# Performance work log

Measured on AMD Instinct MI355X. Metric: run time of the kernel, lower is better.

Reference implementation:

```python
import jax, jax.numpy as jnp
import numpy as np


def _lstm_cell(x, h, c, W_ih, W_hh, b_ih, b_hh):
    # torch.nn.LSTMCell math; gate order i, f, g, o
    gates = x @ W_ih.T + b_ih + h @ W_hh.T + b_hh
    i, f, g, o = jnp.split(gates, 4, axis=-1)
    c_new = jax.nn.sigmoid(f) * c + jax.nn.sigmoid(i) * jnp.tanh(g)
    h_new = jax.nn.sigmoid(o) * jnp.tanh(c_new)
    return h_new, c_new


def setup_inputs() -> dict:
    key = jax.random.key(0)
    ks = jax.random.split(key, 14)
    B, T, F = 16384, 128, 12
    H1, H2 = 64, 128
    s0 = 1.0 / np.sqrt(H1)
    s1 = 1.0 / np.sqrt(H2)
    u = lambda k, shape, s: jax.random.uniform(k, shape, jnp.float32, -s, s)
    return {
        "input_seq": jax.random.normal(ks[0], (B, T, F), jnp.float32),
        "W_ih0": u(ks[1], (4 * H1, F), s0),
        "W_hh0": u(ks[2], (4 * H1, H1), s0),
        "b_ih0": u(ks[3], (4 * H1,), s0),
        "b_hh0": u(ks[4], (4 * H1,), s0),
        "W_ih1": u(ks[5], (4 * H2, H1), s1),
        "W_hh1": u(ks[6], (4 * H2, H2), s1),
        "b_ih1": u(ks[7], (4 * H2,), s1),
        "b_hh1": u(ks[8], (4 * H2,), s1),
        "W_d1": u(ks[9], (H1, H2), s1),
        "b_d1": u(ks[10], (H1,), s1),
        "W_d2": u(ks[11], (1, H1), s0),
        "b_d2": u(ks[12], (1,), s0),
    }


def reference(input_seq, W_ih0, W_hh0, b_ih0, b_hh0,
              W_ih1, W_hh1, b_ih1, b_hh1,
              W_d1, b_d1, W_d2, b_d2):
    B = input_seq.shape[0]
    H1 = W_hh0.shape[1]
    H2 = W_hh1.shape[1]
    dt = input_seq.dtype
    init = (jnp.zeros((B, H1), dt), jnp.zeros((B, H1), dt),
            jnp.zeros((B, H2), dt), jnp.zeros((B, H2), dt))

    def step(carry, x_t):
        h0, c0, h1, c1 = carry
        h0, c0 = _lstm_cell(x_t, h0, c0, W_ih0, W_hh0, b_ih0, b_hh0)
        # dropout is identity in eval mode
        h1, c1 = _lstm_cell(h0, h1, c1, W_ih1, W_hh1, b_ih1, b_hh1)
        return (h0, c0, h1, c1), None

    xs = jnp.swapaxes(input_seq, 0, 1)  # [T, B, F]
    (h0, c0, h1, c1), _ = jax.lax.scan(step, init, xs)
    pred = (h1 @ W_d1.T + b_d1) @ W_d2.T + b_d2  # [B, 1]
    return pred
```

## Files before the change

kernel.cpp:

```cpp
#include <hip/hip_runtime.h>
#include <hip/hip_fp16.h>


#define T_STEPS 128
#define F_IN    12
#define R       32

#define WF0_H8  (16*3*64)
#define WF1_H8  (16*12*64)
#define WH_TOTAL_HALVES ((WF0_H8 + WF1_H8)*8)

typedef _Float16 half8 __attribute__((ext_vector_type(8)));
typedef _Float16 half4 __attribute__((ext_vector_type(4)));
typedef float   floatx4  __attribute__((ext_vector_type(4)));
typedef float   floatx16 __attribute__((ext_vector_type(16)));
typedef int     intx4  __attribute__((ext_vector_type(4)));

__device__ __forceinline__ float vexp2(float x){
  float r; asm("v_exp_f32 %0, %1" : "=v"(r) : "v"(x)); return r;
}
__device__ __forceinline__ float vrcp(float x){
  float r; asm("v_rcp_f32 %0, %1" : "=v"(r) : "v"(x)); return r;
}
__device__ __forceinline__ float sigf(float x){
  return vrcp(1.0f + vexp2(-1.4426950408889634f * x));
}
__device__ __forceinline__ float tanhf_(float x){
  return fmaf(2.0f, vrcp(1.0f + vexp2(-2.8853900817779268f * x)), -1.0f);
}

__device__ __forceinline__ float qpx1(float v){
  return __int_as_float(__builtin_amdgcn_update_dpp(
      0, __float_as_int(v), 0xB1 , 0xF, 0xF, true));
}
__device__ __forceinline__ float qpx2(float v){
  return __int_as_float(__builtin_amdgcn_update_dpp(
      0, __float_as_int(v), 0x4E , 0xF, 0xF, true));
}
__device__ __forceinline__ floatx4 qtrans4(floatx4 s, int g){
  float e0 = qpx1(s[1]), e1 = qpx1(s[0]), e2 = qpx1(s[3]), e3 = qpx1(s[2]);
  const bool lo = (g & 1);
  float m0 = lo ? e0   : s[0];
  float m1 = lo ? s[1] : e1;
  float m2 = lo ? e2   : s[2];
  float m3 = lo ? s[3] : e3;
  float f0 = qpx2(m2), f1 = qpx2(m3), f2 = qpx2(m0), f3 = qpx2(m1);
  const bool hi = (g & 2);
  floatx4 d;
  d[0] = hi ? f0 : m0;
  d[1] = hi ? f1 : m1;
  d[2] = hi ? m2 : f2;
  d[3] = hi ? m3 : f3;
  return d;
}

__global__ void prep_kernel(const float* __restrict__ Wih0, const float* __restrict__ Whh0,
                            const float* __restrict__ bih0, const float* __restrict__ bhh0,
                            const float* __restrict__ Wih1, const float* __restrict__ Whh1,
                            const float* __restrict__ bih1, const float* __restrict__ bhh1,
                            _Float16* __restrict__ wh, float* __restrict__ bs) {
  int tid = blockIdx.x * 256 + threadIdx.x;
  if (tid < WF0_H8) {
    int lane = tid & 63; int kt = (tid >> 6) % 3; int ct = tid / (64*3);
    int p = ct*16 + (lane & 15);
    int col = (p & 3)*64 + (p >> 2);
    int kbase = kt*32 + (lane >> 4)*8;
    #pragma unroll
    for (int j = 0; j < 8; ++j) {
      int k = kbase + j; float w = 0.0f;
      if (k < 12) w = Wih0[col*12 + k];
      else if (k < 76) w = Whh0[col*64 + (k-12)];
      wh[tid*8 + j] = (_Float16)w;
    }
  } else if (tid < WF0_H8 + WF1_H8) {
    int t2 = tid - WF0_H8;
    int lane = t2 & 63; int kt = (t2 >> 6) % 12; int ct = t2 / (64*12);
    int p = ct*32 + (lane & 31);
    int col = (p & 3)*128 + (p >> 2);
    int kbase = kt*16 + (lane >> 5)*8;
    #pragma unroll
    for (int j = 0; j < 8; ++j) {
      int k = kbase + j;
      float w = (k < 64) ? Wih1[col*64 + k] : Whh1[col*128 + (k-64)];
      wh[WF0_H8*8 + t2*8 + j] = (_Float16)w;
    }
  } else if (tid < WF0_H8 + WF1_H8 + 768) {
    int t3 = tid - (WF0_H8 + WF1_H8);
    if (t3 < 256) { int col = (t3 & 3)*64 + (t3 >> 2);  bs[t3] = bih0[col] + bhh0[col]; }
    else { int p1 = t3 - 256; int col = (p1 & 3)*128 + (p1 >> 2); bs[t3] = bih1[col] + bhh1[col]; }
  }
}

__global__ __launch_bounds__(512, 1)
void lstm_kernel(const float* __restrict__ x, const _Float16* __restrict__ wh,
                 const float* __restrict__ bs,
                 const float* __restrict__ Wd1, const float* __restrict__ bd1,
                 const float* __restrict__ Wd2, const float* __restrict__ bd2,
                 float* __restrict__ out) {
  __shared__ __align__(16) _Float16 st0[2*R*128];
  __shared__ __align__(16) _Float16 st1[R*512];
  __shared__ float hbuf[R*132];
  __shared__ float red[R*17];

  const int tid  = threadIdx.x;
  const int w    = tid >> 6;
  const int lane = tid & 63;
  const int l15  = lane & 15;
  const int l31  = lane & 31;
  const int lg   = lane >> 4;
  const int hi5  = lane >> 5;
  const int qg   = lane & 3;
  const int a    = l15 >> 2;
  const int r    = lg*4 + qg;
  const int rowbase = blockIdx.x * R;

  auto st0a = [](int buf, int row, int blk){
    return (buf*R + row)*128 + (((blk ^ (row & 7)) << 3)); };
  auto st0s = [](int buf, int row, int idx){
    return (buf*R + row)*128 + ((((idx >> 3) ^ (row & 7)) << 3) | (idx & 7)); };
  auto st1a = [](int row, int blk){
    return row*512 + (((blk ^ (row & 7)) << 3)); };
  auto st1s = [](int row, int idx){
    return row*512 + ((((idx >> 3) ^ (row & 7)) << 3) | (idx & 7)); };

  const intx4* whi = (const intx4*)wh;
  intx4 wb0i[2][3];
  #pragma unroll
  for (int i = 0; i < 2; ++i)
    #pragma unroll
    for (int kt = 0; kt < 3; ++kt) wb0i[i][kt] = whi[((2*w+i)*3 + kt)*64 + lane];
  intx4 wb1i[2][12];
  #pragma unroll
  for (int i = 0; i < 2; ++i)
    #pragma unroll
    for (int kt = 0; kt < 12; ++kt) wb1i[i][kt] = whi[WF0_H8 + ((2*w+i)*12 + kt)*64 + lane];
  float b0[2], b1[2];
  #pragma unroll
  for (int i = 0; i < 2; ++i) b0[i] = bs[(2*w+i)*16 + l15];
  #pragma unroll
  for (int i = 0; i < 2; ++i) b1[i] = bs[256 + (2*w+i)*32 + l31];

  float c0s[2][2] = {{0.0f,0.0f},{0.0f,0.0f}};
  float c1s[2][4] = {{0.0f,0.0f,0.0f,0.0f},{0.0f,0.0f,0.0f,0.0f}};

  for (int i = tid; i < (2*R*128)/2; i += 512) ((int*)st0)[i] = 0;
  for (int i = tid; i < (R*512)/2;   i += 512) ((int*)st1)[i] = 0;
  __syncthreads();
  const int xr = tid / 3, xq = tid % 3;
  if (tid < 96) {
    float4 v0 = *(const float4*)&x[((size_t)(rowbase + xr)*T_STEPS + 0)*F_IN + xq*4];
    float4 v1 = *(const float4*)&x[((size_t)(rowbase + xr)*T_STEPS + 1)*F_IN + xq*4];
    half4 h40 = {(_Float16)v0.x, (_Float16)v0.y, (_Float16)v0.z, (_Float16)v0.w};
    half4 h41 = {(_Float16)v1.x, (_Float16)v1.y, (_Float16)v1.z, (_Float16)v1.w};
    *(half4*)&st0[st0s(0, xr, xq*4)] = h40;
    *(half4*)&st0[st0s(1, xr, xq*4)] = h41;
  }
  __syncthreads();

  auto do_A = [&](int tt, int i, int mt){
    const int pr = tt & 1;
    const int row16 = mt*16;
    const int ct = 2*w + i;
    floatx4 acc = {b0[i], b0[i], b0[i], b0[i]};
    #pragma unroll
    for (int kt = 0; kt < 3; ++kt) {
      half8 af = *(const half8*)&st0[st0a(pr, row16 + l15, kt*4 + lg)];
      acc = __builtin_amdgcn_mfma_f32_16x16x32_f16(af, __builtin_bit_cast(half8, wb0i[i][kt]), acc, 0, 0, 0);
    }
    floatx4 d = qtrans4(acc, qg);
    float c = fmaf(sigf(d[1]), c0s[i][mt], sigf(d[0]) * tanhf_(d[2]));
    c0s[i][mt] = c;
    float h0v = sigf(d[3]) * tanhf_(c);
    _Float16 hh = (_Float16)h0v;
    const int row = row16 + r;
    const int h0i = 4*ct + a;
    st0[st0s(pr^1, row, 12 + h0i)] = hh;
    st1[st1s(row, pr*64 + h0i)]    = hh;
  };

  auto do_C = [&](int tt, int i){
    const int pr = tt & 1;
    const int ct = 2*w + i;
    floatx16 acc;
    #pragma unroll
    for (int j = 0; j < 16; ++j) acc[j] = b1[i];
    #pragma unroll
    for (int kt = 0; kt < 12; ++kt) {
      const int klog = kt*16 + hi5*8;
      const int idx  = (klog < 64) ? (pr*64 + klog)
                                   : (128 + (pr^1)*128 + (klog - 64));
      half8 af = *(const half8*)&st1[st1a(l31, idx >> 3)];
      acc = __builtin_amdgcn_mfma_f32_32x32x16_f16(af, __builtin_bit_cast(half8, wb1i[i][kt]), acc, 0, 0, 0);
    }
    const int h1w = 8*ct + (l31 >> 2);
    #pragma unroll
    for (int G = 0; G < 4; ++G) {
      floatx4 s = {acc[4*G+0], acc[4*G+1], acc[4*G+2], acc[4*G+3]};
      floatx4 d = qtrans4(s, qg);
      float c = fmaf(sigf(d[1]), c1s[i][G], sigf(d[0]) * tanhf_(d[2]));
      c1s[i][G] = c;
      float h1v = sigf(d[3]) * tanhf_(c);
      const int row = 8*G + 4*hi5 + qg;
      st1[st1s(row, 128 + pr*128 + h1w)] = (_Float16)h1v;
      if (tt == T_STEPS - 1) hbuf[row*132 + h1w] = h1v;
    }
  };

  do_A(0, 0, 0); do_A(0, 0, 1); do_A(0, 1, 0); do_A(0, 1, 1);
  __syncthreads();

  for (int t = 0; t < T_STEPS; t += 2) {
    #pragma unroll
    for (int i = 0; i < 2; ++i) {
      #pragma unroll
      for (int kt = 0; kt < 3; ++kt) asm volatile("" : "+v"(wb0i[i][kt]));
      #pragma unroll
      for (int kt = 0; kt < 12; ++kt) asm volatile("" : "+v"(wb1i[i][kt]));
    }
    asm volatile("" : "+v"(b0[0]), "+v"(b0[1]), "+v"(b1[0]), "+v"(b1[1]));

    #pragma unroll
    for (int hl = 0; hl < 2; ++hl) {
      const int tt = t + hl;
      const int pr = hl;
      float4 xv = {0.0f, 0.0f, 0.0f, 0.0f};
      const bool dopre = (tt + 2 < T_STEPS);
      if (tid < 96 && dopre)
        xv = *(const float4*)&x[((size_t)(rowbase + xr)*T_STEPS + (tt+2))*F_IN + xq*4];

      do_C(tt, 0);
      do_C(tt, 1);
      if (tt + 1 < T_STEPS) {
        do_A(tt+1, 0, 0); do_A(tt+1, 0, 1);
        do_A(tt+1, 1, 0); do_A(tt+1, 1, 1);
      }

      if (tid < 96 && dopre) {
        half4 h4 = {(_Float16)xv.x, (_Float16)xv.y, (_Float16)xv.z, (_Float16)xv.w};
        *(half4*)&st0[st0s(pr, xr, xq*4)] = h4;
      }
      __syncthreads();
    }
  }

  {
    const int hr = tid & 31, jg = tid >> 5;
    float partial = 0.0f;
    #pragma unroll
    for (int jj = 0; jj < 8; ++jj) {
      int j = jg*8 + jj;
      float dacc = bd1[j];
      const float4* wrow = (const float4*)&Wd1[j*128];
      #pragma unroll 8
      for (int k4 = 0; k4 < 32; ++k4) {
        float4 wv = wrow[k4];
        const float4 hv = *(const float4*)&hbuf[hr*132 + k4*4];
        dacc = fmaf(wv.x, hv.x, dacc); dacc = fmaf(wv.y, hv.y, dacc);
        dacc = fmaf(wv.z, hv.z, dacc); dacc = fmaf(wv.w, hv.w, dacc);
      }
      partial = fmaf(Wd2[j], dacc, partial);
    }
    red[hr*17 + jg] = partial;
  }
  __syncthreads();
  if (tid < R) {
    float ssum = bd2[0];
    #pragma unroll
    for (int k = 0; k < 16; ++k) ssum += red[tid*17 + k];
    out[rowbase + tid] = ssum;
  }
}

extern "C" void kernel_launch(void* const* d_in, const int* in_sizes, int n_in,
                              void* d_out, int out_size, void* d_ws, size_t ws_size,
                              hipStream_t stream) {
  const float* x    = (const float*)d_in[0];
  const float* Wih0 = (const float*)d_in[1];
  const float* Whh0 = (const float*)d_in[2];
  const float* bih0 = (const float*)d_in[3];
  const float* bhh0 = (const float*)d_in[4];
  const float* Wih1 = (const float*)d_in[5];
  const float* Whh1 = (const float*)d_in[6];
  const float* bih1 = (const float*)d_in[7];
  const float* bhh1 = (const float*)d_in[8];
  const float* Wd1  = (const float*)d_in[9];
  const float* bd1  = (const float*)d_in[10];
  const float* Wd2  = (const float*)d_in[11];
  const float* bd2  = (const float*)d_in[12];
  float* out = (float*)d_out;

  _Float16* wh  = (_Float16*)d_ws;
  float*    bsv = (float*)((char*)d_ws + (size_t)WH_TOTAL_HALVES * 2);

  prep_kernel<<<63, 256, 0, stream>>>(Wih0, Whh0, bih0, bhh0, Wih1, Whh1, bih1, bhh1, wh, bsv);
  lstm_kernel<<<512, 512, 0, stream>>>(x, wh, bsv, Wd1, bd1, Wd2, bd2, out);
}
```

Baseline: 873.3 us.

## Replace XOR-swizzled LDS layout with padded rows and share A-fragment loads

Drops the XOR swizzle on the shared-memory state buffers and pads the rows instead (136 and 520 halves), so addresses become precomputed bases plus constant offsets. The K ordering of the st1 buffer is also rearranged so h0 and h1 share one contiguous region per parity. Each A-fragment LDS read is now reused for both column tiles, giving two MFMAs per load and halving LDS reads in the recurrent loop. The padding has to keep bank conflicts low on its own, and the reordered K layout must still match the packed weight ordering.

```diff
diff --git a/kernel.cpp b/kernel.cpp
--- a/kernel.cpp
+++ b/kernel.cpp
@@ -5,6 +5,8 @@
 #define T_STEPS 128
 #define F_IN    12
 #define R       32
+#define S0H     136
+#define S1H     520
 
 #define WF0_H8  (16*3*64)
 #define WF1_H8  (16*12*64)
@@ -97,8 +99,8 @@
                  const float* __restrict__ Wd1, const float* __restrict__ bd1,
                  const float* __restrict__ Wd2, const float* __restrict__ bd2,
                  float* __restrict__ out) {
-  __shared__ __align__(16) _Float16 st0[2*R*128];
-  __shared__ __align__(16) _Float16 st1[R*512];
+  __shared__ __align__(16) _Float16 st0[2*R*S0H];
+  __shared__ __align__(16) _Float16 st1[R*S1H];
   __shared__ float hbuf[R*132];
   __shared__ float red[R*17];
 
@@ -111,17 +113,9 @@
   const int hi5  = lane >> 5;
   const int qg   = lane & 3;
   const int a    = l15 >> 2;
+  const int u    = l31 >> 2;
   const int r    = lg*4 + qg;
   const int rowbase = blockIdx.x * R;
-
-  auto st0a = [](int buf, int row, int blk){
-    return (buf*R + row)*128 + (((blk ^ (row & 7)) << 3)); };
-  auto st0s = [](int buf, int row, int idx){
-    return (buf*R + row)*128 + ((((idx >> 3) ^ (row & 7)) << 3) | (idx & 7)); };
-  auto st1a = [](int row, int blk){
-    return row*512 + (((blk ^ (row & 7)) << 3)); };
-  auto st1s = [](int row, int idx){
-    return row*512 + ((((idx >> 3) ^ (row & 7)) << 3) | (idx & 7)); };
 
   const intx4* whi = (const intx4*)wh;
   intx4 wb0i[2][3];
@@ -143,8 +137,14 @@
   float c0s[2][2] = {{0.0f,0.0f},{0.0f,0.0f}};
   float c1s[2][4] = {{0.0f,0.0f,0.0f,0.0f},{0.0f,0.0f,0.0f,0.0f}};
 
-  for (int i = tid; i < (2*R*128)/2; i += 512) ((int*)st0)[i] = 0;
-  for (int i = tid; i < (R*512)/2;   i += 512) ((int*)st1)[i] = 0;
+  const int rdA0 = l15*S0H + lg*8;
+  const int rdA1 = l31*S1H + hi5*8;
+  const int wrH0st0 = r*S0H + 12 + 8*w + a;
+  const int wrH0st1 = r*S1H + 8*w + a;
+  const int wrH1 = (4*hi5 + qg)*S1H + 16*w + u;
+
+  for (int i = tid; i < (2*R*S0H)/2; i += 512) ((int*)st0)[i] = 0;
+  for (int i = tid; i < (R*S1H)/2;   i += 512) ((int*)st1)[i] = 0;
   __syncthreads();
   const int xr = tid / 3, xq = tid % 3;
   if (tid < 96) {
@@ -152,61 +152,68 @@
     float4 v1 = *(const float4*)&x[((size_t)(rowbase + xr)*T_STEPS + 1)*F_IN + xq*4];
     half4 h40 = {(_Float16)v0.x, (_Float16)v0.y, (_Float16)v0.z, (_Float16)v0.w};
     half4 h41 = {(_Float16)v1.x, (_Float16)v1.y, (_Float16)v1.z, (_Float16)v1.w};
-    *(half4*)&st0[st0s(0, xr, xq*4)] = h40;
-    *(half4*)&st0[st0s(1, xr, xq*4)] = h41;
+    *(half4*)&st0[xr*S0H + xq*4]           = h40;
+    *(half4*)&st0[R*S0H + xr*S0H + xq*4]   = h41;
   }
   __syncthreads();
 
-  auto do_A = [&](int tt, int i, int mt){
+  auto do_A = [&](int tt, int mt){
     const int pr = tt & 1;
-    const int row16 = mt*16;
-    const int ct = 2*w + i;
-    floatx4 acc = {b0[i], b0[i], b0[i], b0[i]};
+    const int rbase = rdA0 + pr*(R*S0H) + mt*(16*S0H);
+    floatx4 acc0 = {b0[0], b0[0], b0[0], b0[0]};
+    floatx4 acc1 = {b0[1], b0[1], b0[1], b0[1]};
     #pragma unroll
     for (int kt = 0; kt < 3; ++kt) {
-      half8 af = *(const half8*)&st0[st0a(pr, row16 + l15, kt*4 + lg)];
-      acc = __builtin_amdgcn_mfma_f32_16x16x32_f16(af, __builtin_bit_cast(half8, wb0i[i][kt]), acc, 0, 0, 0);
-    }
-    floatx4 d = qtrans4(acc, qg);
-    float c = fmaf(sigf(d[1]), c0s[i][mt], sigf(d[0]) * tanhf_(d[2]));
-    c0s[i][mt] = c;
-    float h0v = sigf(d[3]) * tanhf_(c);
-    _Float16 hh = (_Float16)h0v;
-    const int row = row16 + r;
-    const int h0i = 4*ct + a;
-    st0[st0s(pr^1, row, 12 + h0i)] = hh;
-    st1[st1s(row, pr*64 + h0i)]    = hh;
+      half8 af = *(const half8*)&st0[rbase + kt*32];
+      acc0 = __builtin_amdgcn_mfma_f32_16x16x32_f16(af, __builtin_bit_cast(half8, wb0i[0][kt]), acc0, 0, 0, 0);
+      acc1 = __builtin_amdgcn_mfma_f32_16x16x32_f16(af, __builtin_bit_cast(half8, wb0i[1][kt]), acc1, 0, 0, 0);
+    }
+    #pragma unroll
+    for (int i = 0; i < 2; ++i) {
+      floatx4 d = qtrans4(i ? acc1 : acc0, qg);
+      float c = fmaf(sigf(d[1]), c0s[i][mt], sigf(d[0]) * tanhf_(d[2]));
+      c0s[i][mt] = c;
+      float h0v = sigf(d[3]) * tanhf_(c);
+      _Float16 hh = (_Float16)h0v;
+      st0[wrH0st0 + (pr^1)*(R*S0H) + mt*(16*S0H) + 4*i] = hh;
+      st1[wrH0st1 + mt*(16*S1H) + pr*192 + 4*i]          = hh;
+    }
   };
 
-  auto do_C = [&](int tt, int i){
+  auto do_C = [&](int tt){
     const int pr = tt & 1;
-    const int ct = 2*w + i;
-    floatx16 acc;
-    #pragma unroll
-    for (int j = 0; j < 16; ++j) acc[j] = b1[i];
+    const int rbase = rdA1 + pr*192;
+    floatx16 acc0, acc1;
+    #pragma unroll
+    for (int j = 0; j < 16; ++j) { acc0[j] = b1[0]; acc1[j] = b1[1]; }
     #pragma unroll
     for (int kt = 0; kt < 12; ++kt) {
-      const int klog = kt*16 + hi5*8;
-      const int idx  = (klog < 64) ? (pr*64 + klog)
-                                   : (128 + (pr^1)*128 + (klog - 64));
-      half8 af = *(const half8*)&st1[st1a(l31, idx >> 3)];
-      acc = __builtin_amdgcn_mfma_f32_32x32x16_f16(af, __builtin_bit_cast(half8, wb1i[i][kt]), acc, 0, 0, 0);
-    }
-    const int h1w = 8*ct + (l31 >> 2);
-    #pragma unroll
-    for (int G = 0; G < 4; ++G) {
-      floatx4 s = {acc[4*G+0], acc[4*G+1], acc[4*G+2], acc[4*G+3]};
-      floatx4 d = qtrans4(s, qg);
-      float c = fmaf(sigf(d[1]), c1s[i][G], sigf(d[0]) * tanhf_(d[2]));
-      c1s[i][G] = c;
-      float h1v = sigf(d[3]) * tanhf_(c);
-      const int row = 8*G + 4*hi5 + qg;
-      st1[st1s(row, 128 + pr*128 + h1w)] = (_Float16)h1v;
-      if (tt == T_STEPS - 1) hbuf[row*132 + h1w] = h1v;
+      half8 af = *(const half8*)&st1[rbase + kt*16];
+      acc0 = __builtin_amdgcn_mfma_f32_32x32x16_f16(af, __builtin_bit_cast(half8, wb1i[0][kt]), acc0, 0, 0, 0);
+      acc1 = __builtin_amdgcn_mfma_f32_32x32x16_f16(af, __builtin_bit_cast(half8, wb1i[1][kt]), acc1, 0, 0, 0);
+    }
+    const int wbase = wrH1 + (pr ? 64 : 256);
+    #pragma unroll
+    for (int i = 0; i < 2; ++i) {
+      #pragma unroll
+      for (int G = 0; G < 4; ++G) {
+        floatx4 s;
+        if (i) { s[0]=acc1[4*G+0]; s[1]=acc1[4*G+1]; s[2]=acc1[4*G+2]; s[3]=acc1[4*G+3]; }
+        else   { s[0]=acc0[4*G+0]; s[1]=acc0[4*G+1]; s[2]=acc0[4*G+2]; s[3]=acc0[4*G+3]; }
+        floatx4 d = qtrans4(s, qg);
+        float c = fmaf(sigf(d[1]), c1s[i][G], sigf(d[0]) * tanhf_(d[2]));
+        c1s[i][G] = c;
+        float h1v = sigf(d[3]) * tanhf_(c);
+        st1[wbase + G*(8*S1H) + 8*i] = (_Float16)h1v;
+        if (tt == T_STEPS - 1) {
+          const int row = 8*G + 4*hi5 + qg;
+          hbuf[row*132 + 16*w + 8*i + u] = h1v;
+        }
+      }
     }
   };
 
-  do_A(0, 0, 0); do_A(0, 0, 1); do_A(0, 1, 0); do_A(0, 1, 1);
+  do_A(0, 0); do_A(0, 1);
   __syncthreads();
 
   for (int t = 0; t < T_STEPS; t += 2) {
@@ -228,16 +235,12 @@
       if (tid < 96 && dopre)
         xv = *(const float4*)&x[((size_t)(rowbase + xr)*T_STEPS + (tt+2))*F_IN + xq*4];
 
-      do_C(tt, 0);
-      do_C(tt, 1);
-      if (tt + 1 < T_STEPS) {
-        do_A(tt+1, 0, 0); do_A(tt+1, 0, 1);
-        do_A(tt+1, 1, 0); do_A(tt+1, 1, 1);
-      }
+      do_C(tt);
+      if (tt + 1 < T_STEPS) { do_A(tt+1, 0); do_A(tt+1, 1); }
 
       if (tid < 96 && dopre) {
         half4 h4 = {(_Float16)xv.x, (_Float16)xv.y, (_Float16)xv.z, (_Float16)xv.w};
-        *(half4*)&st0[st0s(pr, xr, xq*4)] = h4;
+        *(half4*)&st0[pr*(R*S0H) + xr*S0H + xq*4] = h4;
       }
       __syncthreads();
     }
```

New measurement: 840.2 us. -3.8%, faster.
